# Performance work log

Hardware: AMD Instinct MI355X
Metric: run time of the kernel (lower is better)

The kernel has to match this reference:

```python
import jax, jax.numpy as jnp
import numpy as np

D, H, B, T = 256, 512, 16, 512

def setup_inputs() -> dict:
    key = jax.random.key(0)
    ks = jax.random.split(key, 4)
    x = jax.random.normal(ks[0], (B, T, D), dtype=jnp.float32)
    W_w = jax.random.normal(ks[1], (4 * H, D), dtype=jnp.float32) / np.sqrt(D)
    U_w = jax.random.normal(ks[2], (4 * H, H), dtype=jnp.float32) / np.sqrt(H)
    V_w = jax.random.normal(ks[3], (H, D * H), dtype=jnp.float32) / np.sqrt(D * H)
    return {
        "x": x,
        "W_w": W_w, "W_b": jnp.zeros((4 * H,), jnp.float32),
        "U_w": U_w, "U_b": jnp.zeros((4 * H,), jnp.float32),
        "V_w": V_w, "V_b": jnp.zeros((H,), jnp.float32),
    }

def reference(x, W_w, W_b, U_w, U_b, V_w, V_b):
    Bz, Tz, Dz = x.shape
    Hz = U_w.shape[1]
    # Precompute input projections for all timesteps in one big GEMM: (B,T,4H)
    wx_all = jnp.einsum('btd,gd->btg', x, W_w) + W_b

    def step(carry, inputs):
        h, c = carry
        xt, wx = inputs  # xt: (B,D), wx: (B,4H)
        gates = wx + h @ U_w.T + U_b
        i, f, o, g = jnp.split(gates, 4, axis=-1)
        i, f, o, g = jax.nn.sigmoid(i), jax.nn.sigmoid(f), jax.nn.sigmoid(o), jnp.tanh(g)
        # outer product x_t (B,D) x h (B,H) -> (B, D*H), row-major like torch reshape
        mult = (xt[:, :, None] * h[:, None, :]).reshape(Bz, Dz * Hz)
        m = jnp.tanh(mult @ V_w.T + V_b)
        c = f * c + i * g + 0.1 * m
        h = o * jnp.tanh(c)
        return (h, c), h

    h0 = jnp.zeros((Bz, Hz), x.dtype)
    c0 = jnp.zeros((Bz, Hz), x.dtype)
    (hT, cT), outs = jax.lax.scan(
        step, (h0, c0), (jnp.swapaxes(x, 0, 1), jnp.swapaxes(wx_all, 0, 1)))
    outs = jnp.swapaxes(outs, 0, 1)  # (B,T,H)
    return outs, (hT, cT)
```

## Files before the change

kernel.cpp:

```cpp
#include <hip/hip_runtime.h>
#include <cstdint>
#include <cstddef>

#define Dk 256
#define Hk 512
#define Bk 16
#define Tk 512
#define Gk 2048
#define NVk 262144
#define NBLK 256

typedef __bf16 bf16;
typedef __bf16 bf16x8 __attribute__((ext_vector_type(8)));
typedef float  f32x4  __attribute__((ext_vector_type(4)));
typedef const __attribute__((address_space(1))) void* gvp;
typedef __attribute__((address_space(3))) void* lvp;

__device__ __forceinline__ float bflo(unsigned u) {
  u <<= 16; return __builtin_bit_cast(float, u);
}
__device__ __forceinline__ float bfhi(unsigned u) {
  u &= 0xffff0000u; return __builtin_bit_cast(float, u);
}

__device__ __forceinline__ int ld_rlx(const int* p) {
  return __hip_atomic_load(p, __ATOMIC_RELAXED, __HIP_MEMORY_SCOPE_AGENT);
}
__device__ __forceinline__ void st_rlx(int* p, int v) {
  __hip_atomic_store(p, v, __ATOMIC_RELAXED, __HIP_MEMORY_SCOPE_AGENT);
}
#define VMWAIT asm volatile("s_waitcnt vmcnt(0)" ::: "memory")

__global__ __launch_bounds__(256) void cvt_f32_bf16(const float* __restrict__ in,
                                                    bf16* __restrict__ out, int n8) {
  int i = blockIdx.x * 256 + threadIdx.x;
  if (i >= n8) return;
  const float4* p = reinterpret_cast<const float4*>(in) + (size_t)i * 2;
  float4 a = p[0], b = p[1];
  bf16x8 v;
  v[0] = (bf16)a.x; v[1] = (bf16)a.y; v[2] = (bf16)a.z; v[3] = (bf16)a.w;
  v[4] = (bf16)b.x; v[5] = (bf16)b.y; v[6] = (bf16)b.z; v[7] = (bf16)b.w;
  *reinterpret_cast<bf16x8*>(out + (size_t)i * 8) = v;
}

__global__ __launch_bounds__(256) void pack_V(const float* __restrict__ Vw,
                                              bf16* __restrict__ V2p) {
  int n = blockIdx.x * 256 + threadIdx.x;
  int j = n >> 9, hp = n & 511;
  const float* src = Vw + (size_t)j * 131072 + hp;
  for (int kb = 0; kb < 32; ++kb) {
    bf16x8 v;
#pragma unroll
    for (int r = 0; r < 8; ++r) v[r] = (bf16)src[(size_t)(kb * 8 + r) * 512];
    *reinterpret_cast<bf16x8*>(V2p + ((size_t)kb * NVk + n) * 8) = v;
  }
}

__global__ __launch_bounds__(256) void pack_W(const float* __restrict__ Ww,
                                              bf16* __restrict__ Wp) {
  int g = blockIdx.x * 256 + threadIdx.x;
  const float* src = Ww + (size_t)g * 256;
  for (int kb = 0; kb < 32; ++kb) {
    bf16x8 v;
#pragma unroll
    for (int r = 0; r < 8; ++r) v[r] = (bf16)src[kb * 8 + r];
    *reinterpret_cast<bf16x8*>(Wp + ((size_t)kb * Gk + g) * 8) = v;
  }
}

__global__ __launch_bounds__(256) void pack_x(const float* __restrict__ x,
                                              bf16* __restrict__ xp) {
  int row = blockIdx.x * 256 + threadIdx.x;
  const float* src = x + (size_t)row * 256;
  for (int kb = 0; kb < 32; ++kb) {
    bf16x8 v;
#pragma unroll
    for (int r = 0; r < 8; ++r) v[r] = (bf16)src[kb * 8 + r];
    *reinterpret_cast<bf16x8*>(xp + ((size_t)kb * 8192 + row) * 8) = v;
  }
}

__global__ __launch_bounds__(256) void init_state(bf16* __restrict__ hbuf,
                                                  float* __restrict__ cws,
                                                  int* __restrict__ bar) {
  int i = blockIdx.x * 256 + threadIdx.x;
  if (i < 16384) hbuf[i] = (bf16)0.f;
  if (i < 8192)  cws[i]  = 0.f;
  if (i < 2048)  bar[i]  = 0;
}

template <bool BF16_OUT>
__global__ __launch_bounds__(256) void gemm128(const bf16* __restrict__ Ap,
                                               const bf16* __restrict__ Bp,
                                               float* __restrict__ outF,
                                               bf16* __restrict__ outB,
                                               const float* __restrict__ bias,
                                               const float* __restrict__ bias2,
                                               int N, int Mtot,
                                               int t0, int tcMask, int tcShift,
                                               int swzShift) {
  __shared__ uint4 a_sm[512];
  __shared__ uint4 b_sm[512];
  int tid = threadIdx.x;
  int lane = tid & 63, w = tid >> 6;
  int quad = lane >> 4, l15 = lane & 15;
  int wm = w >> 1, wn = w & 1;
  int m0, n0;
  if (swzShift >= 0) {
    int id = blockIdx.x;
    int r = id & 7, q = id >> 3;
    m0 = (q & ((1 << swzShift) - 1)) << 7;
    n0 = (r + ((q >> swzShift) << 3)) << 7;
  } else {
    m0 = blockIdx.x << 7; n0 = blockIdx.y << 7;
  }

  f32x4 acc[4][4];
#pragma unroll
  for (int i = 0; i < 4; ++i)
#pragma unroll
    for (int j = 0; j < 4; ++j) acc[i][j] = (f32x4){0.f, 0.f, 0.f, 0.f};

  int gm0 = m0 + lane, gm1 = m0 + 64 + lane;
  int xr0 = ((gm0 >> tcShift) << 9) + t0 + (gm0 & tcMask);
  int xr1 = ((gm1 >> tcShift) << 9) + t0 + (gm1 & tcMask);
  const uint4* gA = reinterpret_cast<const uint4*>(Ap);
  const uint4* gB = reinterpret_cast<const uint4*>(Bp);

  const bf16x8* aptr = reinterpret_cast<const bf16x8*>(a_sm);
  const bf16x8* bptr = reinterpret_cast<const bf16x8*>(b_sm);

  for (int kk = 0; kk < 8; ++kk) {
    size_t kbg = (size_t)(kk * 4 + w);
    __builtin_amdgcn_global_load_lds((gvp)(gA + kbg * Mtot + xr0),
                                     (lvp)(&a_sm[w * 128]), 16, 0, 0);
    __builtin_amdgcn_global_load_lds((gvp)(gA + kbg * Mtot + xr1),
                                     (lvp)(&a_sm[w * 128 + 64]), 16, 0, 0);
    __builtin_amdgcn_global_load_lds((gvp)(gB + kbg * N + n0 + lane),
                                     (lvp)(&b_sm[w * 128]), 16, 0, 0);
    __builtin_amdgcn_global_load_lds((gvp)(gB + kbg * N + n0 + 64 + lane),
                                     (lvp)(&b_sm[w * 128 + 64]), 16, 0, 0);
    __syncthreads();
    bf16x8 af[4], bfr[4];
#pragma unroll
    for (int i = 0; i < 4; ++i) af[i]  = aptr[quad * 128 + wm * 64 + i * 16 + l15];
#pragma unroll
    for (int j = 0; j < 4; ++j) bfr[j] = bptr[quad * 128 + wn * 64 + j * 16 + l15];
#pragma unroll
    for (int i = 0; i < 4; ++i)
#pragma unroll
      for (int j = 0; j < 4; ++j)
        acc[i][j] = __builtin_amdgcn_mfma_f32_16x16x32_bf16(af[i], bfr[j], acc[i][j], 0, 0, 0);
    __syncthreads();
  }

  if constexpr (BF16_OUT) {
    __shared__ bf16 c_sm[128 * 136];
#pragma unroll
    for (int i = 0; i < 4; ++i) {
      int row = wm * 64 + i * 16 + quad * 4;
#pragma unroll
      for (int j = 0; j < 4; ++j) {
        int col = wn * 64 + j * 16 + l15;
        f32x4 v = acc[i][j];
#pragma unroll
        for (int r = 0; r < 4; ++r)
          c_sm[(row + r) * 136 + col] = (bf16)v[r];
      }
    }
    __syncthreads();
    int rr = tid >> 4, cc = (tid & 15) * 8;
#pragma unroll
    for (int k = 0; k < 8; ++k) {
      int row = k * 16 + rr;
      bf16x8 v = *reinterpret_cast<const bf16x8*>(&c_sm[row * 136 + cc]);
      *reinterpret_cast<bf16x8*>(&outB[(size_t)(m0 + row) * N + n0 + cc]) = v;
    }
  } else {
#pragma unroll
    for (int i = 0; i < 4; ++i) {
      int row = m0 + wm * 64 + i * 16 + quad * 4;
#pragma unroll
      for (int j = 0; j < 4; ++j) {
        int col = n0 + wn * 64 + j * 16 + l15;
        f32x4 v = acc[i][j];
        float bv = bias[col] + bias2[col];
#pragma unroll
        for (int r = 0; r < 4; ++r)
          outF[(size_t)(row + r) * N + col] = v[r] + bv;
      }
    }
  }
}

__global__ __launch_bounds__(256) void scan_step3(
    const bf16* __restrict__ A, int trel, int Tc,
    const bf16* __restrict__ Ubf, const float* __restrict__ wx,
    const float* __restrict__ Vb,
    const bf16* __restrict__ hprev, bf16* __restrict__ hnext,
    float* __restrict__ cst, float* __restrict__ out, int t) {
  __shared__ bf16 U_s[4 * Hk];
  __shared__ float gate_s[64];
  __shared__ float m_s[16];
  int tid = threadIdx.x;
  int j = blockIdx.x;
  int b = tid >> 4, sm = tid & 15;

  const bf16* Ar = A + ((size_t)b * Tc + trel) * NVk + (size_t)j * Hk;
  uint4 av[4];
#pragma unroll
  for (int i = 0; i < 4; ++i)
    av[i] = *reinterpret_cast<const uint4*>(Ar + i * 128 + sm * 8);

  uint4 hv[4];
#pragma unroll
  for (int i = 0; i < 4; ++i)
    hv[i] = *reinterpret_cast<const uint4*>(hprev + b * Hk + i * 128 + sm * 8);

  {
    int r = tid >> 6, e = (tid & 63) * 8;
    *reinterpret_cast<uint4*>(U_s + r * Hk + e) =
        *reinterpret_cast<const uint4*>(Ubf + ((size_t)r * Hk + j) * Hk + e);
  }
  __syncthreads();

  float hf[4][8];
#pragma unroll
  for (int i = 0; i < 4; ++i) {
    unsigned ux = hv[i].x, uy = hv[i].y, uz = hv[i].z, uw = hv[i].w;
    hf[i][0] = bflo(ux); hf[i][1] = bfhi(ux);
    hf[i][2] = bflo(uy); hf[i][3] = bfhi(uy);
    hf[i][4] = bflo(uz); hf[i][5] = bfhi(uz);
    hf[i][6] = bflo(uw); hf[i][7] = bfhi(uw);
  }

  float accs[5] = {0.f, 0.f, 0.f, 0.f, 0.f};
  const uint4* Uq = reinterpret_cast<const uint4*>(U_s);
#pragma unroll
  for (int i = 0; i < 4; ++i) {
#pragma unroll
    for (int q = 0; q < 4; ++q) {
      uint4 u = Uq[q * 64 + i * 16 + sm];
      accs[q] += bflo(u.x) * hf[i][0] + bfhi(u.x) * hf[i][1]
               + bflo(u.y) * hf[i][2] + bfhi(u.y) * hf[i][3]
               + bflo(u.z) * hf[i][4] + bfhi(u.z) * hf[i][5]
               + bflo(u.w) * hf[i][6] + bfhi(u.w) * hf[i][7];
    }
    uint4 a = av[i];
    accs[4] += bflo(a.x) * hf[i][0] + bfhi(a.x) * hf[i][1]
             + bflo(a.y) * hf[i][2] + bfhi(a.y) * hf[i][3]
             + bflo(a.z) * hf[i][4] + bfhi(a.z) * hf[i][5]
             + bflo(a.w) * hf[i][6] + bfhi(a.w) * hf[i][7];
  }
#pragma unroll
  for (int d = 1; d < 16; d <<= 1) {
#pragma unroll
    for (int k = 0; k < 5; ++k) accs[k] += __shfl_xor(accs[k], d);
  }
  if (sm == 0) {
    const float* wxr = wx + ((size_t)b * Tk + t) * Gk + j;
#pragma unroll
    for (int q = 0; q < 4; ++q) gate_s[q * 16 + b] = accs[q] + wxr[q * Hk];
    m_s[b] = accs[4];
  }
  __syncthreads();

  if (tid < 16) {
    int bb = tid;
    float gi = gate_s[bb], gf = gate_s[16 + bb];
    float go = gate_s[32 + bb], gg = gate_s[48 + bb];
    float iv = 1.f / (1.f + __expf(-gi));
    float fv = 1.f / (1.f + __expf(-gf));
    float ov = 1.f / (1.f + __expf(-go));
    float gv = tanhf(gg);
    float mv = tanhf(m_s[bb] + Vb[j]);
    int idx = bb * Hk + j;
    float c = fv * cst[idx] + iv * gv + 0.1f * mv;
    cst[idx] = c;
    float h = ov * tanhf(c);
    hnext[idx] = (bf16)h;
    out[((size_t)bb * Tk + t) * Hk + j] = h;
    if (t == Tk - 1) {
      out[(size_t)Bk * Tk * Hk + idx] = h;
      out[(size_t)Bk * Tk * Hk + Bk * Hk + idx] = c;
    }
  }
}

__device__ __forceinline__ void gbar_slots(int* bar, int target) {
  __syncthreads();
  int tid = threadIdx.x;
  if (blockIdx.x == 0) {
    if (tid < 64) {
      if (tid == 0) { VMWAIT; st_rlx(bar + 0, target); }
      for (;;) {
        bool ok = ld_rlx(bar + tid)       >= target &&
                  ld_rlx(bar + 64 + tid)  >= target &&
                  ld_rlx(bar + 128 + tid) >= target &&
                  ld_rlx(bar + 192 + tid) >= target;
        if (__all(ok)) break;
        __builtin_amdgcn_s_sleep(2);
      }
      if (tid == 0) st_rlx(bar + 1024, target);
    }
  } else if (tid == 0) {
    VMWAIT;
    st_rlx(bar + blockIdx.x, target);
    while (ld_rlx(bar + 1024) < target) __builtin_amdgcn_s_sleep(2);
  }
  __syncthreads();
}

__global__ __launch_bounds__(256) void scan_persist2(
    const bf16* __restrict__ A, int Tc, int c0,
    const bf16* __restrict__ Ubf, const float* __restrict__ wx,
    const float* __restrict__ Vb, bf16* __restrict__ hbuf,
    float* __restrict__ cst, float* __restrict__ out, int* __restrict__ bar) {
  __shared__ bf16 U_s[8 * 512];
  __shared__ float gate_s[128];
  __shared__ float m_s[32];
  int tid = threadIdx.x;
  int j0 = blockIdx.x * 2;
  int b = tid >> 4, sm = tid & 15;

  {
    int r = tid >> 5;
    int q = r >> 1, jj = r & 1;
    int e = (tid & 31) * 8;
#pragma unroll
    for (int k = 0; k < 2; ++k)
      *reinterpret_cast<uint4*>(U_s + r * 512 + e + k * 256) =
          *reinterpret_cast<const uint4*>(
              Ubf + ((size_t)(q * 512 + j0 + jj)) * 512 + e + k * 256);
  }
  float c_reg = 0.f, vb = 0.f;
  if (tid < 32) {
    int bb = tid & 15, jj = tid >> 4;
    c_reg = cst[bb * Hk + j0 + jj];
    vb = Vb[j0 + jj];
  }
  __syncthreads();

  const uint4* Aq = reinterpret_cast<const uint4*>(A);
  const uint4* Uq = reinterpret_cast<const uint4*>(U_s);
  size_t abase = (size_t)(b * Tc) * (NVk / 8) + (size_t)j0 * 64 + sm;

  uint4 avA[2][4], avB[2][4];
#pragma unroll
  for (int jj = 0; jj < 2; ++jj)
#pragma unroll
    for (int i = 0; i < 4; ++i) avA[jj][i] = Aq[abase + jj * 64 + i * 16];

  for (int trel = 0; trel < Tc; ++trel) {
    int t = c0 + trel;
    const bf16* hprev = hbuf + (t & 1) * 8192;
    bf16* hnext = hbuf + ((t + 1) & 1) * 8192;

    unsigned long long hw[4][2];
    const unsigned long long* Hd =
        reinterpret_cast<const unsigned long long*>(hprev);
#pragma unroll
    for (int i = 0; i < 4; ++i)
#pragma unroll
      for (int k = 0; k < 2; ++k)
        hw[i][k] = __hip_atomic_load(Hd + b * 128 + i * 32 + sm * 2 + k,
                                     __ATOMIC_RELAXED, __HIP_MEMORY_SCOPE_AGENT);

    float wxq[2][4] = {{0.f, 0.f, 0.f, 0.f}, {0.f, 0.f, 0.f, 0.f}};
    if (sm == 0) {
      const float* wxr = wx + ((size_t)b * Tk + t) * Gk + j0;
#pragma unroll
      for (int jj = 0; jj < 2; ++jj)
#pragma unroll
        for (int q = 0; q < 4; ++q) wxq[jj][q] = wxr[q * Hk + jj];
    }

    float accs[2][5] = {{0.f, 0.f, 0.f, 0.f, 0.f}, {0.f, 0.f, 0.f, 0.f, 0.f}};
#pragma unroll
    for (int i = 0; i < 4; ++i) {
      float hf[8];
      unsigned lo0 = (unsigned)hw[i][0], hi0 = (unsigned)(hw[i][0] >> 32);
      unsigned lo1 = (unsigned)hw[i][1], hi1 = (unsigned)(hw[i][1] >> 32);
      hf[0] = bflo(lo0); hf[1] = bfhi(lo0);
      hf[2] = bflo(hi0); hf[3] = bfhi(hi0);
      hf[4] = bflo(lo1); hf[5] = bfhi(lo1);
      hf[6] = bflo(hi1); hf[7] = bfhi(hi1);
#pragma unroll
      for (int jj = 0; jj < 2; ++jj) {
#pragma unroll
        for (int q = 0; q < 4; ++q) {
          uint4 u = Uq[(q * 2 + jj) * 64 + i * 16 + sm];
          accs[jj][q] += bflo(u.x) * hf[0] + bfhi(u.x) * hf[1]
                       + bflo(u.y) * hf[2] + bfhi(u.y) * hf[3]
                       + bflo(u.z) * hf[4] + bfhi(u.z) * hf[5]
                       + bflo(u.w) * hf[6] + bfhi(u.w) * hf[7];
        }
        uint4 a = avA[jj][i];
        accs[jj][4] += bflo(a.x) * hf[0] + bfhi(a.x) * hf[1]
                     + bflo(a.y) * hf[2] + bfhi(a.y) * hf[3]
                     + bflo(a.z) * hf[4] + bfhi(a.z) * hf[5]
                     + bflo(a.w) * hf[6] + bfhi(a.w) * hf[7];
      }
    }

    if (trel + 1 < Tc) {
      size_t nb = abase + (size_t)(trel + 1) * (NVk / 8);
#pragma unroll
      for (int jj = 0; jj < 2; ++jj)
#pragma unroll
        for (int i = 0; i < 4; ++i) avB[jj][i] = Aq[nb + jj * 64 + i * 16];
    }

#pragma unroll
    for (int d = 1; d < 16; d <<= 1) {
#pragma unroll
      for (int jj = 0; jj < 2; ++jj)
#pragma unroll
        for (int k = 0; k < 5; ++k) accs[jj][k] += __shfl_xor(accs[jj][k], d);
    }
    if (sm == 0) {
#pragma unroll
      for (int jj = 0; jj < 2; ++jj) {
#pragma unroll
        for (int q = 0; q < 4; ++q)
          gate_s[jj * 64 + q * 16 + b] = accs[jj][q] + wxq[jj][q];
        m_s[jj * 16 + b] = accs[jj][4];
      }
    }
    __syncthreads();

    if (tid < 32) {
      int bb = tid & 15, jj = tid >> 4;
      float gi = gate_s[jj * 64 + bb];
      float gf = gate_s[jj * 64 + 16 + bb];
      float go = gate_s[jj * 64 + 32 + bb];
      float gg = gate_s[jj * 64 + 48 + bb];
      float iv = 1.f / (1.f + __expf(-gi));
      float fv = 1.f / (1.f + __expf(-gf));
      float ov = 1.f / (1.f + __expf(-go));
      float gv = tanhf(gg);
      float mv = tanhf(m_s[jj * 16 + bb] + vb);
      float c = fv * c_reg + iv * gv + 0.1f * mv;
      c_reg = c;
      float h = ov * tanhf(c);
      float hOther = __shfl_down(h, 16);
      if (jj == 0) {
        unsigned lo = (unsigned)__builtin_bit_cast(unsigned short, (bf16)h);
        unsigned hi = (unsigned)__builtin_bit_cast(unsigned short, (bf16)hOther);
        unsigned u = lo | (hi << 16);
        unsigned* hp = reinterpret_cast<unsigned*>(hnext) + ((bb * Hk + j0) >> 1);
        __hip_atomic_store(hp, u, __ATOMIC_RELAXED, __HIP_MEMORY_SCOPE_AGENT);
      }
      out[((size_t)bb * Tk + t) * Hk + j0 + jj] = h;
      if (t == Tk - 1) {
        out[(size_t)Bk * Tk * Hk + bb * Hk + j0 + jj] = h;
        out[(size_t)Bk * Tk * Hk + Bk * Hk + bb * Hk + j0 + jj] = c;
      }
    }

    if (trel + 1 < Tc) {
      gbar_slots(bar, t + 1);
#pragma unroll
      for (int jj = 0; jj < 2; ++jj)
#pragma unroll
        for (int i = 0; i < 4; ++i) avA[jj][i] = avB[jj][i];
    }
  }
  if (tid < 32) cst[(tid & 15) * Hk + j0 + (tid >> 4)] = c_reg;
}

extern "C" void kernel_launch(void* const* d_in, const int* in_sizes, int n_in,
                              void* d_out, int out_size, void* d_ws, size_t ws_size,
                              hipStream_t stream) {
  const float* x  = (const float*)d_in[0];
  const float* Ww = (const float*)d_in[1];
  const float* Wb = (const float*)d_in[2];
  const float* Uw = (const float*)d_in[3];
  const float* Ub = (const float*)d_in[4];
  const float* Vw = (const float*)d_in[5];
  const float* Vb = (const float*)d_in[6];
  float* out = (float*)d_out;

  char* ws = (char*)d_ws;
  size_t off = 0;
  auto alloc = [&](size_t bytes) -> void* {
    void* p = ws + off;
    off = (off + bytes + 255) & ~(size_t)255;
    return p;
  };
  bf16*  xp   = (bf16*)alloc((size_t)Bk * Tk * Dk * 2);
  bf16*  V2p  = (bf16*)alloc((size_t)32 * NVk * 8 * 2);
  bf16*  Wp   = (bf16*)alloc((size_t)32 * Gk * 8 * 2);
  bf16*  Ubf  = (bf16*)alloc((size_t)Gk * Hk * 2);
  float* wx   = (float*)alloc((size_t)Bk * Tk * Gk * 4);
  bf16*  hbuf = (bf16*)alloc((size_t)16384 * 2);
  float* cws  = (float*)alloc((size_t)8192 * 4);
  int*   bar  = (int*)alloc(2048 * sizeof(int));
  size_t fixedBytes = off;

  int Tc = 512;
  while (Tc > 8 && fixedBytes + (size_t)Bk * Tc * Hk * Hk * 2 > ws_size) Tc >>= 1;
  bf16* A_ws = (bf16*)alloc((size_t)Bk * Tc * Hk * Hk * 2);
  int tcShift = 31 - __builtin_clz((unsigned)Tc);
  int mt = Bk * Tc / 128;
  int mtShift = 31 - __builtin_clz((unsigned)mt);

  pack_x<<<32, 256, 0, stream>>>(x, xp);
  cvt_f32_bf16<<<512, 256, 0, stream>>>(Uw, Ubf, 131072);
  pack_V<<<1024, 256, 0, stream>>>(Vw, V2p);
  pack_W<<<8, 256, 0, stream>>>(Ww, Wp);
  init_state<<<64, 256, 0, stream>>>(hbuf, cws, bar);

  gemm128<false><<<dim3(64, 16), 256, 0, stream>>>(xp, Wp, wx, nullptr, Wb, Ub,
                                                   Gk, 8192, 0, 511, 9, -1);

  for (int c0 = 0; c0 < Tk; c0 += Tc) {
    gemm128<true><<<dim3(mt * (NVk / 128)), 256, 0, stream>>>(
        xp, V2p, nullptr, A_ws, nullptr, nullptr, NVk, 8192, c0, Tc - 1,
        tcShift, mtShift);

    int TcV = Tc, c0V = c0;
    void* args[] = {(void*)&A_ws, (void*)&TcV, (void*)&c0V, (void*)&Ubf,
                    (void*)&wx, (void*)&Vb, (void*)&hbuf, (void*)&cws,
                    (void*)&out, (void*)&bar};
    hipError_t e = hipLaunchCooperativeKernel((const void*)scan_persist2,
                                              dim3(NBLK), dim3(256), args, 0, stream);
    if (e != hipSuccess) {
      for (int t = c0; t < c0 + Tc; ++t)
        scan_step3<<<512, 256, 0, stream>>>(
            A_ws, t - c0, Tc, Ubf, wx, Vb,
            hbuf + (t & 1) * 8192, hbuf + ((t + 1) & 1) * 8192,
            cws, out, t);
    }
  }
}
```

Baseline: 6.269 ms.

## Tile precomputed A in time-contiguous blocks, tree grid barrier, prefetch wx

The GEMM epilogue now writes the bf16 A matrix in 128-column tiles with time-contiguous rows, staged through half-size shared memory with a rotated column swizzle. The scan kernels read A in this new layout, so each block's per-step slice is contiguous along time and consecutive steps fall close together in memory. The single-master grid barrier is replaced by a two-level tree barrier over groups of 16 blocks, meant to cut polling contention on one block. The wx gate inputs are prefetched one step ahead into registers, like the A prefetch, taking their load latency off the serial path.

Result: no change. 6.263 ms (-0.1%).

```diff
diff --git a/kernel.cpp b/kernel.cpp
--- a/kernel.cpp
+++ b/kernel.cpp
@@ -155,26 +155,38 @@
   }
 
   if constexpr (BF16_OUT) {
-    __shared__ bf16 c_sm[128 * 136];
-#pragma unroll
-    for (int i = 0; i < 4; ++i) {
-      int row = wm * 64 + i * 16 + quad * 4;
-#pragma unroll
-      for (int j = 0; j < 4; ++j) {
-        int col = wn * 64 + j * 16 + l15;
-        f32x4 v = acc[i][j];
-#pragma unroll
-        for (int r = 0; r < 4; ++r)
-          c_sm[(row + r) * 136 + col] = (bf16)v[r];
-      }
-    }
-    __syncthreads();
-    int rr = tid >> 4, cc = (tid & 15) * 8;
-#pragma unroll
-    for (int k = 0; k < 8; ++k) {
-      int row = k * 16 + rr;
-      bf16x8 v = *reinterpret_cast<const bf16x8*>(&c_sm[row * 136 + cc]);
-      *reinterpret_cast<bf16x8*>(&outB[(size_t)(m0 + row) * N + n0 + cc]) = v;
+    __shared__ bf16 c_sm[64 * 136];
+    int Mc = 128 << swzShift;
+    size_t tbase = ((size_t)(n0 >> 7) * Mc + m0) * 128;
+#pragma unroll
+    for (int p = 0; p < 2; ++p) {
+      if (wm == p) {
+#pragma unroll
+        for (int i = 0; i < 4; ++i) {
+          int rl = i * 16 + quad * 4;
+          int cshift = quad * 16;
+#pragma unroll
+          for (int j = 0; j < 4; ++j) {
+            int col = wn * 64 + j * 16 + l15;
+            int cs = (col + cshift) & 127;
+            f32x4 v = acc[i][j];
+#pragma unroll
+            for (int r = 0; r < 4; ++r)
+              c_sm[(rl + r) * 136 + cs] = (bf16)v[r];
+          }
+        }
+      }
+      __syncthreads();
+      int rr = tid >> 4, cc = (tid & 15) * 8;
+      int rshift = ((rr >> 2) & 3) * 16;
+      int csr = (cc + rshift) & 127;
+#pragma unroll
+      for (int k = 0; k < 4; ++k) {
+        int rl = k * 16 + rr;
+        bf16x8 v = *reinterpret_cast<const bf16x8*>(&c_sm[rl * 136 + csr]);
+        *reinterpret_cast<bf16x8*>(&outB[tbase + (size_t)(p * 64 + rl) * 128 + cc]) = v;
+      }
+      __syncthreads();
     }
   } else {
 #pragma unroll
@@ -205,12 +217,13 @@
   int tid = threadIdx.x;
   int j = blockIdx.x;
   int b = tid >> 4, sm = tid & 15;
-
-  const bf16* Ar = A + ((size_t)b * Tc + trel) * NVk + (size_t)j * Hk;
+  size_t Mc = (size_t)Bk * Tc;
+
+  const uint4* Aq = reinterpret_cast<const uint4*>(A);
   uint4 av[4];
 #pragma unroll
   for (int i = 0; i < 4; ++i)
-    av[i] = *reinterpret_cast<const uint4*>(Ar + i * 128 + sm * 8);
+    av[i] = Aq[((size_t)(j * 4 + i) * Mc + (size_t)b * Tc + trel) * 16 + sm];
 
   uint4 hv[4];
 #pragma unroll
@@ -287,26 +300,25 @@
   }
 }
 
-__device__ __forceinline__ void gbar_slots(int* bar, int target) {
+__device__ __forceinline__ void gbar_tree(int* bar, int target) {
   __syncthreads();
   int tid = threadIdx.x;
-  if (blockIdx.x == 0) {
-    if (tid < 64) {
-      if (tid == 0) { VMWAIT; st_rlx(bar + 0, target); }
-      for (;;) {
-        bool ok = ld_rlx(bar + tid)       >= target &&
-                  ld_rlx(bar + 64 + tid)  >= target &&
-                  ld_rlx(bar + 128 + tid) >= target &&
-                  ld_rlx(bar + 192 + tid) >= target;
-        if (__all(ok)) break;
-        __builtin_amdgcn_s_sleep(2);
-      }
-      if (tid == 0) st_rlx(bar + 1024, target);
-    }
-  } else if (tid == 0) {
-    VMWAIT;
-    st_rlx(bar + blockIdx.x, target);
-    while (ld_rlx(bar + 1024) < target) __builtin_amdgcn_s_sleep(2);
+  int bid = blockIdx.x, g = bid >> 4;
+  if (tid == 0) { VMWAIT; st_rlx(bar + bid, target); }
+  if ((bid & 15) == 0) {
+    if (tid < 16) {
+      while (!__all(ld_rlx(bar + g * 16 + tid) >= target))
+        __builtin_amdgcn_s_sleep(1);
+      if (tid == 0) st_rlx(bar + 256 + g * 32, target);
+      while (!__all(ld_rlx(bar + 256 + tid * 32) >= target))
+        __builtin_amdgcn_s_sleep(1);
+      if (tid == 0) st_rlx(bar + 768 + g * 32, target);
+    }
+  } else {
+    if (tid == 0) {
+      while (ld_rlx(bar + 768 + g * 32) < target)
+        __builtin_amdgcn_s_sleep(1);
+    }
   }
   __syncthreads();
 }
@@ -343,13 +355,24 @@
 
   const uint4* Aq = reinterpret_cast<const uint4*>(A);
   const uint4* Uq = reinterpret_cast<const uint4*>(U_s);
-  size_t abase = (size_t)(b * Tc) * (NVk / 8) + (size_t)j0 * 64 + sm;
+  size_t Mc16 = (size_t)(Bk * Tc) * 16;
+  size_t abase = (size_t)(j0 * 4) * Mc16 + (size_t)(b * Tc) * 16 + sm;
 
   uint4 avA[2][4], avB[2][4];
 #pragma unroll
   for (int jj = 0; jj < 2; ++jj)
 #pragma unroll
-    for (int i = 0; i < 4; ++i) avA[jj][i] = Aq[abase + jj * 64 + i * 16];
+    for (int i = 0; i < 4; ++i)
+      avA[jj][i] = Aq[abase + (size_t)(jj * 4 + i) * Mc16];
+
+  float wxqA[2][4] = {{0.f,0.f,0.f,0.f},{0.f,0.f,0.f,0.f}}, wxqB[2][4];
+  if (sm == 0) {
+    const float* wxr = wx + ((size_t)b * Tk + c0) * Gk + j0;
+#pragma unroll
+    for (int jj = 0; jj < 2; ++jj)
+#pragma unroll
+      for (int q = 0; q < 4; ++q) wxqA[jj][q] = wxr[q * Hk + jj];
+  }
 
   for (int trel = 0; trel < Tc; ++trel) {
     int t = c0 + trel;
@@ -365,15 +388,6 @@
       for (int k = 0; k < 2; ++k)
         hw[i][k] = __hip_atomic_load(Hd + b * 128 + i * 32 + sm * 2 + k,
                                      __ATOMIC_RELAXED, __HIP_MEMORY_SCOPE_AGENT);
-
-    float wxq[2][4] = {{0.f, 0.f, 0.f, 0.f}, {0.f, 0.f, 0.f, 0.f}};
-    if (sm == 0) {
-      const float* wxr = wx + ((size_t)b * Tk + t) * Gk + j0;
-#pragma unroll
-      for (int jj = 0; jj < 2; ++jj)
-#pragma unroll
-        for (int q = 0; q < 4; ++q) wxq[jj][q] = wxr[q * Hk + jj];
-    }
 
     float accs[2][5] = {{0.f, 0.f, 0.f, 0.f, 0.f}, {0.f, 0.f, 0.f, 0.f, 0.f}};
 #pragma unroll
@@ -404,11 +418,19 @@
     }
 
     if (trel + 1 < Tc) {
-      size_t nb = abase + (size_t)(trel + 1) * (NVk / 8);
+      size_t nb = abase + (size_t)(trel + 1) * 16;
 #pragma unroll
       for (int jj = 0; jj < 2; ++jj)
 #pragma unroll
-        for (int i = 0; i < 4; ++i) avB[jj][i] = Aq[nb + jj * 64 + i * 16];
+        for (int i = 0; i < 4; ++i)
+          avB[jj][i] = Aq[nb + (size_t)(jj * 4 + i) * Mc16];
+      if (sm == 0) {
+        const float* wxr = wx + ((size_t)b * Tk + t + 1) * Gk + j0;
+#pragma unroll
+        for (int jj = 0; jj < 2; ++jj)
+#pragma unroll
+          for (int q = 0; q < 4; ++q) wxqB[jj][q] = wxr[q * Hk + jj];
+      }
     }
 
 #pragma unroll
@@ -423,7 +445,7 @@
       for (int jj = 0; jj < 2; ++jj) {
 #pragma unroll
         for (int q = 0; q < 4; ++q)
-          gate_s[jj * 64 + q * 16 + b] = accs[jj][q] + wxq[jj][q];
+          gate_s[jj * 64 + q * 16 + b] = accs[jj][q] + wxqA[jj][q];
         m_s[jj * 16 + b] = accs[jj][4];
       }
     }
@@ -459,11 +481,14 @@
     }
 
     if (trel + 1 < Tc) {
-      gbar_slots(bar, t + 1);
-#pragma unroll
-      for (int jj = 0; jj < 2; ++jj)
+      gbar_tree(bar, t + 1);
+#pragma unroll
+      for (int jj = 0; jj < 2; ++jj) {
 #pragma unroll
         for (int i = 0; i < 4; ++i) avA[jj][i] = avB[jj][i];
+#pragma unroll
+        for (int q = 0; q < 4; ++q) wxqA[jj][q] = wxqB[jj][q];
+      }
     }
   }
   if (tid < 32) cst[(tid & 15) * Hk + j0 + (tid >> 4)] = c_reg;
```
